# Kernel tuning notes

Hardware: AMD Instinct MI355X
Metric: run time of the kernel (lower is better)

The kernel has to match this reference:

```python
import jax, jax.numpy as jnp
import numpy as np

N = 50000
E = 800000
IN_CH = 128
HID = 32
HEADS = 8
OUT_CH = 64
NEG_SLOPE = 0.2  # PyG GATConv default leaky_relu slope


def setup_inputs() -> dict:
    key = jax.random.key(0)
    ks = jax.random.split(key, 16)
    x = jax.random.normal(ks[0], (N, IN_CH), dtype=jnp.float32)
    edge_index = jax.random.randint(ks[1], (2, E), 0, N, dtype=jnp.int64)
    s = 0.1
    return {
        "x": x,
        "edge_index": edge_index,
        # layer 1: in -> (HEADS, HID), concat
        "W1": jax.random.normal(ks[2], (IN_CH, HEADS * HID), dtype=jnp.float32) * s,
        "att_src1": jax.random.normal(ks[3], (HEADS, HID), dtype=jnp.float32) * s,
        "att_dst1": jax.random.normal(ks[4], (HEADS, HID), dtype=jnp.float32) * s,
        "b1": jnp.zeros((HEADS * HID,), dtype=jnp.float32),
        # layer 2: HEADS*HID -> (HEADS, HID), concat
        "W2": jax.random.normal(ks[5], (HEADS * HID, HEADS * HID), dtype=jnp.float32) * s,
        "att_src2": jax.random.normal(ks[6], (HEADS, HID), dtype=jnp.float32) * s,
        "att_dst2": jax.random.normal(ks[7], (HEADS, HID), dtype=jnp.float32) * s,
        "b2": jnp.zeros((HEADS * HID,), dtype=jnp.float32),
        # layer 3: HEADS*HID -> (1, OUT_CH), no concat (heads=1)
        "W3": jax.random.normal(ks[8], (HEADS * HID, OUT_CH), dtype=jnp.float32) * s,
        "att_src3": jax.random.normal(ks[9], (1, OUT_CH), dtype=jnp.float32) * s,
        "att_dst3": jax.random.normal(ks[10], (1, OUT_CH), dtype=jnp.float32) * s,
        "b3": jnp.zeros((OUT_CH,), dtype=jnp.float32),
    }


def gat_conv(x, src, dst, W, a_src, a_dst, b, heads, ch, concat):
    n = x.shape[0]
    h = (x @ W).reshape(n, heads, ch)                      # [N,H,C]
    alpha_src = jnp.sum(h * a_src, axis=-1)                # [N,H]
    alpha_dst = jnp.sum(h * a_dst, axis=-1)                # [N,H]
    logits = jax.nn.leaky_relu(alpha_src[src] + alpha_dst[dst], NEG_SLOPE)  # [E,H]
    # numerically stable softmax over edges grouped by destination node
    m = jax.ops.segment_max(logits, dst, num_segments=n)   # [N,H]
    m = jnp.where(jnp.isfinite(m), m, 0.0)
    e = jnp.exp(logits - m[dst])                           # [E,H]
    denom = jax.ops.segment_sum(e, dst, num_segments=n)    # [N,H]
    alpha = e / (denom[dst] + 1e-16)                       # [E,H]
    # weighted scatter-aggregate of source features
    out = jax.ops.segment_sum(alpha[:, :, None] * h[src], dst, num_segments=n)  # [N,H,C]
    out = out.reshape(n, heads * ch) if concat else out.mean(axis=1)
    return out + b


def reference(x, edge_index, W1, att_src1, att_dst1, b1,
              W2, att_src2, att_dst2, b2, W3, att_src3, att_dst3, b3):
    src, dst = edge_index[0], edge_index[1]
    h = jax.nn.elu(gat_conv(x, src, dst, W1, att_src1, att_dst1, b1, HEADS, HID, True))
    h = jax.nn.elu(gat_conv(h, src, dst, W2, att_src2, att_dst2, b2, HEADS, HID, True))
    out = gat_conv(h, src, dst, W3, att_src3, att_dst3, b3, 1, OUT_CH, False)
    return out
```

## Files before the change

kernel.cpp:

```cpp
#include <hip/hip_runtime.h>
#include <hip/hip_bf16.h>
#include <stdint.h>

#define NNODES 50000
#define NEDGES 800000

typedef float f32x4 __attribute__((ext_vector_type(4)));
typedef short short8 __attribute__((ext_vector_type(8)));

__device__ __forceinline__ ushort f2bf(float f) {
  uint32_t u = __float_as_uint(f);
  u += 0x7fff + ((u >> 16) & 1);
  return (ushort)(u >> 16);
}
__device__ __forceinline__ float bf2f(ushort h) {
  return __uint_as_float(((uint32_t)h) << 16);
}
__device__ __forceinline__ float bflo(uint32_t u) { return __uint_as_float(u << 16); }
__device__ __forceinline__ float bfhi(uint32_t u) { return __uint_as_float(u & 0xffff0000u); }

__device__ __forceinline__ void gload_lds16(const void* g, void* l) {
  __builtin_amdgcn_global_load_lds(
      (const __attribute__((address_space(1))) uint32_t*)g,
      (__attribute__((address_space(3))) uint32_t*)l, 16, 0, 0);
}

__global__ __launch_bounds__(256) void gemm_wide(
    const ushort* __restrict__ Ah, const ushort* __restrict__ Al,
    const ushort* __restrict__ Bh, const ushort* __restrict__ Bl,
    const float* __restrict__ a_src, const float* __restrict__ a_dst,
    float* __restrict__ as_out, float* __restrict__ ad_out,
    ushort* __restrict__ Cout, int M, int K) {
  __shared__ ushort AsH[64 * 32];
  __shared__ ushort AsL[64 * 32];
  __shared__ ushort BsH[256 * 32];
  __shared__ ushort BsL[256 * 32];

  const int t = threadIdx.x;
  const int w = t >> 6, ln = t & 63;
  const int row0 = blockIdx.x * 64;
  const int wr = (w >> 1) * 32, wc = (w & 1) * 128;

  f32x4 acc[2][8] = {};

  const int nkt = K >> 5;
  for (int kt = 0; kt < nkt; ++kt) {
    const int k0 = kt << 5;
    {
      int rloc = w * 16 + (ln >> 2);
      int sl = ln & 3;
      int sg = sl ^ ((rloc ^ (rloc >> 2)) & 3);
      int grow = row0 + rloc; grow = grow < M ? grow : M - 1;
      size_t go = (size_t)grow * K + k0 + sg * 8;
      gload_lds16(Ah + go, AsH + w * 512);
      gload_lds16(Al + go, AsL + w * 512);
    }
    #pragma unroll
    for (int i = 0; i < 4; ++i) {
      int rloc = w * 64 + i * 16 + (ln >> 2);
      int sl = ln & 3;
      int sg = sl ^ ((rloc ^ (rloc >> 2)) & 3);
      size_t go = (size_t)rloc * K + k0 + sg * 8;
      gload_lds16(Bh + go, BsH + (w * 64 + i * 16) * 32);
      gload_lds16(Bl + go, BsL + (w * 64 + i * 16) * 32);
    }
    __syncthreads();

    short8 ah[2], al[2], bh[8], bl[8];
    #pragma unroll
    for (int i = 0; i < 2; ++i) {
      int row = wr + i * 16 + (ln & 15);
      int slot = (ln >> 4) ^ ((row ^ (row >> 2)) & 3);
      int off = row * 32 + slot * 8;
      ah[i] = *(const short8*)(AsH + off);
      al[i] = *(const short8*)(AsL + off);
    }
    #pragma unroll
    for (int j = 0; j < 8; ++j) {
      int col = wc + j * 16 + (ln & 15);
      int slot = (ln >> 4) ^ ((col ^ (col >> 2)) & 3);
      int off = col * 32 + slot * 8;
      bh[j] = *(const short8*)(BsH + off);
      bl[j] = *(const short8*)(BsL + off);
    }
    #pragma unroll
    for (int i = 0; i < 2; ++i)
      #pragma unroll
      for (int j = 0; j < 8; ++j) {
        acc[i][j] = __builtin_amdgcn_mfma_f32_16x16x32_bf16(ah[i], bh[j], acc[i][j], 0, 0, 0);
        acc[i][j] = __builtin_amdgcn_mfma_f32_16x16x32_bf16(al[i], bh[j], acc[i][j], 0, 0, 0);
        acc[i][j] = __builtin_amdgcn_mfma_f32_16x16x32_bf16(ah[i], bl[j], acc[i][j], 0, 0, 0);
      }
    __syncthreads();
  }

  const int lx = ln & 15, g = ln >> 4;

  #pragma unroll
  for (int i = 0; i < 2; ++i)
    #pragma unroll
    for (int j = 0; j < 8; ++j)
      #pragma unroll
      for (int r = 0; r < 4; ++r) {
        int grow = row0 + wr + i * 16 + g * 4 + r;
        int gcol = wc + j * 16 + lx;
        if (grow < M) Cout[(size_t)grow * 256 + gcol] = f2bf(acc[i][j][r]);
      }

  const int hbase = wc >> 5;
  float avs[8], avd[8];
  #pragma unroll
  for (int j = 0; j < 8; ++j) {
    avs[j] = a_src[wc + j * 16 + lx];
    avd[j] = a_dst[wc + j * 16 + lx];
  }
  #pragma unroll
  for (int i = 0; i < 2; ++i)
    #pragma unroll
    for (int r = 0; r < 4; ++r) {
      float ps[4] = {0.f, 0.f, 0.f, 0.f}, pd[4] = {0.f, 0.f, 0.f, 0.f};
      #pragma unroll
      for (int j = 0; j < 8; ++j) {
        float v = acc[i][j][r];
        ps[j >> 1] += v * avs[j];
        pd[j >> 1] += v * avd[j];
      }
      #pragma unroll
      for (int m = 1; m < 16; m <<= 1)
        #pragma unroll
        for (int q = 0; q < 4; ++q) {
          ps[q] += __shfl_xor(ps[q], m);
          pd[q] += __shfl_xor(pd[q], m);
        }
      if (lx == 0) {
        int grow = row0 + wr + i * 16 + g * 4 + r;
        if (grow < M) {
          #pragma unroll
          for (int q = 0; q < 4; ++q) {
            as_out[grow * 8 + hbase + q] = ps[q];
            ad_out[grow * 8 + hbase + q] = pd[q];
          }
        }
      }
    }
}

__global__ __launch_bounds__(256) void gemm_mfma3(
    const ushort* __restrict__ Ah, const ushort* __restrict__ Al,
    const ushort* __restrict__ Bh, const ushort* __restrict__ Bl,
    const float* __restrict__ a_src, const float* __restrict__ a_dst,
    float* __restrict__ as_out, float* __restrict__ ad_out,
    ushort* __restrict__ Cout, int M, int K, int Ncols) {
  __shared__ ushort AsH[128 * 64];
  __shared__ ushort AsL[128 * 64];
  __shared__ ushort BsH[64 * 64];
  __shared__ ushort BsL[64 * 64];
  __shared__ float redS[2][128], redD[2][128];

  const int t = threadIdx.x;
  const int w = t >> 6, ln = t & 63;
  const int row0 = blockIdx.y * 128;
  const int col0 = blockIdx.x * 64;
  const int wr = (w >> 1) * 64, wc = (w & 1) * 32;

  f32x4 acc[4][2] = {};

  const int nkt = K >> 6;
  for (int kt = 0; kt < nkt; ++kt) {
    const int k0 = kt << 6;
    #pragma unroll
    for (int i = 0; i < 4; ++i) {
      int row8 = w * 4 + i;
      int rloc = row8 * 8 + (ln >> 3);
      int sslot = (ln & 7) ^ (rloc & 7);
      int grow = row0 + rloc; grow = grow < M ? grow : M - 1;
      size_t go = (size_t)grow * K + k0 + sslot * 8;
      gload_lds16(Ah + go, AsH + row8 * 512);
      gload_lds16(Al + go, AsL + row8 * 512);
    }
    #pragma unroll
    for (int i = 0; i < 2; ++i) {
      int row8 = w * 2 + i;
      int rloc = row8 * 8 + (ln >> 3);
      int sslot = (ln & 7) ^ (rloc & 7);
      size_t go = (size_t)(col0 + rloc) * K + k0 + sslot * 8;
      gload_lds16(Bh + go, BsH + row8 * 512);
      gload_lds16(Bl + go, BsL + row8 * 512);
    }
    __syncthreads();

    #pragma unroll
    for (int ks = 0; ks < 2; ++ks) {
      short8 ah[4], al[4], bh[2], bl[2];
      #pragma unroll
      for (int i = 0; i < 4; ++i) {
        int row = wr + i * 16 + (ln & 15);
        int slot = (ks * 4 + (ln >> 4)) ^ (row & 7);
        int off = row * 64 + slot * 8;
        ah[i] = *(const short8*)(AsH + off);
        al[i] = *(const short8*)(AsL + off);
      }
      #pragma unroll
      for (int j = 0; j < 2; ++j) {
        int col = wc + j * 16 + (ln & 15);
        int slot = (ks * 4 + (ln >> 4)) ^ (col & 7);
        int off = col * 64 + slot * 8;
        bh[j] = *(const short8*)(BsH + off);
        bl[j] = *(const short8*)(BsL + off);
      }
      #pragma unroll
      for (int i = 0; i < 4; ++i)
        #pragma unroll
        for (int j = 0; j < 2; ++j) {
          acc[i][j] = __builtin_amdgcn_mfma_f32_16x16x32_bf16(ah[i], bh[j], acc[i][j], 0, 0, 0);
          acc[i][j] = __builtin_amdgcn_mfma_f32_16x16x32_bf16(al[i], bh[j], acc[i][j], 0, 0, 0);
          acc[i][j] = __builtin_amdgcn_mfma_f32_16x16x32_bf16(ah[i], bl[j], acc[i][j], 0, 0, 0);
        }
    }
    __syncthreads();
  }

  const int lx = ln & 15, g = ln >> 4;

  #pragma unroll
  for (int i = 0; i < 4; ++i)
    #pragma unroll
    for (int j = 0; j < 2; ++j)
      #pragma unroll
      for (int r = 0; r < 4; ++r) {
        int grow = row0 + wr + i * 16 + g * 4 + r;
        int gcol = col0 + wc + j * 16 + lx;
        if (grow < M) Cout[(size_t)grow * Ncols + gcol] = f2bf(acc[i][j][r]);
      }

  float avs[2], avd[2];
  #pragma unroll
  for (int j = 0; j < 2; ++j) {
    avs[j] = a_src[wc + j * 16 + lx];
    avd[j] = a_dst[wc + j * 16 + lx];
  }
  #pragma unroll
  for (int i = 0; i < 4; ++i)
    #pragma unroll
    for (int r = 0; r < 4; ++r) {
      float ps = 0.f, pd = 0.f;
      #pragma unroll
      for (int j = 0; j < 2; ++j) {
        float v = acc[i][j][r];
        ps += v * avs[j];
        pd += v * avd[j];
      }
      #pragma unroll
      for (int m = 1; m < 16; m <<= 1) {
        ps += __shfl_xor(ps, m);
        pd += __shfl_xor(pd, m);
      }
      if (lx == 0) {
        int lrow = wr + i * 16 + g * 4 + r;
        redS[w & 1][lrow] = ps;
        redD[w & 1][lrow] = pd;
      }
    }
  __syncthreads();
  if (t < 128) {
    int grow = row0 + t;
    if (grow < M) {
      as_out[grow] = redS[0][t] + redS[1][t];
      ad_out[grow] = redD[0][t] + redD[1][t];
    }
  }
}

__global__ void cvt_split(const float* __restrict__ in, ushort* __restrict__ hi,
                          ushort* __restrict__ lo, int n4) {
  int idx = blockIdx.x * blockDim.x + threadIdx.x;
  if (idx >= n4) return;
  float4 v = ((const float4*)in)[idx];
  ushort4 h, l;
  h.x = f2bf(v.x); l.x = f2bf(v.x - bf2f(h.x));
  h.y = f2bf(v.y); l.y = f2bf(v.y - bf2f(h.y));
  h.z = f2bf(v.z); l.z = f2bf(v.z - bf2f(h.z));
  h.w = f2bf(v.w); l.w = f2bf(v.w - bf2f(h.w));
  ((ushort4*)hi)[idx] = h;
  ((ushort4*)lo)[idx] = l;
}

__global__ void cvt_w(const float* __restrict__ W, ushort* __restrict__ th,
                      ushort* __restrict__ tl, int K, int N) {
  int idx = blockIdx.x * blockDim.x + threadIdx.x;
  if (idx >= K * N) return;
  int k = idx / N, c = idx - k * N;
  float f = W[idx];
  ushort h = f2bf(f);
  th[(size_t)c * K + k] = h;
  tl[(size_t)c * K + k] = f2bf(f - bf2f(h));
}

__global__ void deg_kernel(const int* __restrict__ dst, int* __restrict__ deg, int E) {
  int e = blockIdx.x * blockDim.x + threadIdx.x;
  if (e < E) atomicAdd(&deg[dst[e]], 1);
}

__global__ __launch_bounds__(256) void scan_partial(const int* __restrict__ deg,
                                                    int* __restrict__ rowptr,
                                                    int* __restrict__ blocksum, int n) {
  __shared__ int sdata[256];
  int t = threadIdx.x;
  int base = blockIdx.x * 1024 + t * 4;
  int v[4], s = 0;
  #pragma unroll
  for (int i = 0; i < 4; ++i) {
    v[i] = (base + i < n) ? deg[base + i] : 0;
    s += v[i];
  }
  sdata[t] = s;
  __syncthreads();
  for (int off = 1; off < 256; off <<= 1) {
    int x = (t >= off) ? sdata[t - off] : 0;
    __syncthreads();
    sdata[t] += x;
    __syncthreads();
  }
  int run = sdata[t] - s;
  #pragma unroll
  for (int i = 0; i < 4; ++i) {
    if (base + i < n) rowptr[base + i] = run;
    run += v[i];
  }
  if (t == 255) blocksum[blockIdx.x] = sdata[255];
}

__global__ __launch_bounds__(256) void scan_blocksums(int* __restrict__ blocksum, int nb) {
  __shared__ int sdata[256];
  int t = threadIdx.x;
  int v = (t < nb) ? blocksum[t] : 0;
  sdata[t] = v;
  __syncthreads();
  for (int off = 1; off < 256; off <<= 1) {
    int x = (t >= off) ? sdata[t - off] : 0;
    __syncthreads();
    sdata[t] += x;
    __syncthreads();
  }
  if (t < nb) blocksum[t] = sdata[t] - v;
}

__global__ void scan_add(int* __restrict__ rowptr, const int* __restrict__ blocksum,
                         int* __restrict__ cursor, int n, int E) {
  int idx = blockIdx.x * blockDim.x + threadIdx.x;
  if (idx < n) {
    rowptr[idx] += blocksum[idx >> 10];
    cursor[idx] = 0;
  }
  if (idx == n) rowptr[n] = E;
}

__global__ void scatter_kernel(const int* __restrict__ src, const int* __restrict__ dst,
                               const int* __restrict__ rowptr, int* __restrict__ cursor,
                               int* __restrict__ col_src, int E) {
  int e = blockIdx.x * blockDim.x + threadIdx.x;
  if (e >= E) return;
  int d = dst[e];
  int pos = rowptr[d] + atomicAdd(&cursor[d], 1);
  col_src[pos] = src[e];
}

__global__ __launch_bounds__(256) void aggr_bf(
    const int* __restrict__ rowptr, const int* __restrict__ col_src,
    const ushort* __restrict__ h, const float* __restrict__ as_,
    const float* __restrict__ ad_, const float* __restrict__ bias,
    ushort* __restrict__ oh, ushort* __restrict__ ol, int n) {
  int d = blockIdx.x * 4 + (threadIdx.x >> 6);
  if (d >= n) return;
  int lane = threadIdx.x & 63;
  int c0 = lane * 4;
  int hd = lane >> 3;
  float ad_d = ad_[d * 8 + hd];
  float a0 = 0.f, a1 = 0.f, a2 = 0.f, a3 = 0.f, denom = 0.f;
  int beg = rowptr[d], end = rowptr[d + 1];
  int i = beg;
  for (; i + 2 <= end; i += 2) {
    int s0 = col_src[i], s1 = col_src[i + 1];
    float l0 = as_[s0 * 8 + hd] + ad_d;
    float l1 = as_[s1 * 8 + hd] + ad_d;
    uint2 v0 = *(const uint2*)(h + (size_t)s0 * 256 + c0);
    uint2 v1 = *(const uint2*)(h + (size_t)s1 * 256 + c0);
    l0 = (l0 > 0.f) ? l0 : 0.2f * l0;
    l1 = (l1 > 0.f) ? l1 : 0.2f * l1;
    float e0 = __expf(l0), e1 = __expf(l1);
    denom += e0 + e1;
    a0 += e0 * bflo(v0.x) + e1 * bflo(v1.x);
    a1 += e0 * bfhi(v0.x) + e1 * bfhi(v1.x);
    a2 += e0 * bflo(v0.y) + e1 * bflo(v1.y);
    a3 += e0 * bfhi(v0.y) + e1 * bfhi(v1.y);
  }
  if (i < end) {
    int s = col_src[i];
    float l = as_[s * 8 + hd] + ad_d;
    l = (l > 0.f) ? l : 0.2f * l;
    float ev = __expf(l);
    denom += ev;
    uint2 v = *(const uint2*)(h + (size_t)s * 256 + c0);
    a0 += ev * bflo(v.x);
    a1 += ev * bfhi(v.x);
    a2 += ev * bflo(v.y);
    a3 += ev * bfhi(v.y);
  }
  float inv = 1.f / (denom + 1e-16f);
  float v0 = a0 * inv + bias[c0 + 0];
  float v1 = a1 * inv + bias[c0 + 1];
  float v2 = a2 * inv + bias[c0 + 2];
  float v3 = a3 * inv + bias[c0 + 3];
  v0 = (v0 > 0.f) ? v0 : expm1f(v0);
  v1 = (v1 > 0.f) ? v1 : expm1f(v1);
  v2 = (v2 > 0.f) ? v2 : expm1f(v2);
  v3 = (v3 > 0.f) ? v3 : expm1f(v3);
  ushort4 hh, ll;
  hh.x = f2bf(v0); ll.x = f2bf(v0 - bf2f(hh.x));
  hh.y = f2bf(v1); ll.y = f2bf(v1 - bf2f(hh.y));
  hh.z = f2bf(v2); ll.z = f2bf(v2 - bf2f(hh.z));
  hh.w = f2bf(v3); ll.w = f2bf(v3 - bf2f(hh.w));
  *(ushort4*)(oh + (size_t)d * 256 + c0) = hh;
  *(ushort4*)(ol + (size_t)d * 256 + c0) = ll;
}

__global__ __launch_bounds__(256) void aggr_f3(
    const int* __restrict__ rowptr, const int* __restrict__ col_src,
    const ushort* __restrict__ h, const float* __restrict__ as_,
    const float* __restrict__ ad_, const float* __restrict__ bias,
    float* __restrict__ outp, int n) {
  int wid = (blockIdx.x * 256 + threadIdx.x) >> 6;
  int d = wid * 4 + ((threadIdx.x >> 4) & 3);
  if (d >= n) return;
  int l = threadIdx.x & 15;
  int c0 = l * 4;
  float ad_d = ad_[d];
  float a0 = 0.f, a1 = 0.f, a2 = 0.f, a3 = 0.f, denom = 0.f;
  int beg = rowptr[d], end = rowptr[d + 1];
  int i = beg;
  for (; i + 2 <= end; i += 2) {
    int s0 = col_src[i], s1 = col_src[i + 1];
    float l0 = as_[s0] + ad_d;
    float l1 = as_[s1] + ad_d;
    uint2 v0 = *(const uint2*)(h + (size_t)s0 * 64 + c0);
    uint2 v1 = *(const uint2*)(h + (size_t)s1 * 64 + c0);
    l0 = (l0 > 0.f) ? l0 : 0.2f * l0;
    l1 = (l1 > 0.f) ? l1 : 0.2f * l1;
    float e0 = __expf(l0), e1 = __expf(l1);
    denom += e0 + e1;
    a0 += e0 * bflo(v0.x) + e1 * bflo(v1.x);
    a1 += e0 * bfhi(v0.x) + e1 * bfhi(v1.x);
    a2 += e0 * bflo(v0.y) + e1 * bflo(v1.y);
    a3 += e0 * bfhi(v0.y) + e1 * bfhi(v1.y);
  }
  if (i < end) {
    int s = col_src[i];
    float lg = as_[s] + ad_d;
    lg = (lg > 0.f) ? lg : 0.2f * lg;
    float ev = __expf(lg);
    denom += ev;
    uint2 v = *(const uint2*)(h + (size_t)s * 64 + c0);
    a0 += ev * bflo(v.x);
    a1 += ev * bfhi(v.x);
    a2 += ev * bflo(v.y);
    a3 += ev * bfhi(v.y);
  }
  float inv = 1.f / (denom + 1e-16f);
  float4 r;
  r.x = a0 * inv + bias[c0 + 0];
  r.y = a1 * inv + bias[c0 + 1];
  r.z = a2 * inv + bias[c0 + 2];
  r.w = a3 * inv + bias[c0 + 3];
  *(float4*)(outp + (size_t)d * 64 + c0) = r;
}


extern "C" void kernel_launch(void* const* d_in, const int* in_sizes, int n_in,
                              void* d_out, int out_size, void* d_ws, size_t ws_size,
                              hipStream_t stream) {
  const float* x   = (const float*)d_in[0];
  const int*   ei  = (const int*)d_in[1];
  const float* W1  = (const float*)d_in[2];
  const float* aS1 = (const float*)d_in[3];
  const float* aD1 = (const float*)d_in[4];
  const float* b1  = (const float*)d_in[5];
  const float* W2  = (const float*)d_in[6];
  const float* aS2 = (const float*)d_in[7];
  const float* aD2 = (const float*)d_in[8];
  const float* b2  = (const float*)d_in[9];
  const float* W3  = (const float*)d_in[10];
  const float* aS3 = (const float*)d_in[11];
  const float* aD3 = (const float*)d_in[12];
  const float* b3  = (const float*)d_in[13];

  const int* srcp = ei;
  const int* dstp = ei + NEDGES;

  char* base = (char*)d_ws;
  size_t o = 0;
  ushort* hbf  = (ushort*)(base + o); o += 25600000;
  ushort* fh   = (ushort*)(base + o); o += 25600000;
  ushort* fl   = (ushort*)(base + o); o += 25600000;
  ushort* f1h  = (ushort*)(base + o); o += 12800000;
  ushort* f1l  = (ushort*)(base + o); o += 12800000;
  float*  as_  = (float*)(base + o);  o += 1600000;
  float*  ad_  = (float*)(base + o);  o += 1600000;
  ushort* w1h  = (ushort*)(base + o); o += 65536;
  ushort* w1l  = (ushort*)(base + o); o += 65536;
  ushort* w2h  = (ushort*)(base + o); o += 131072;
  ushort* w2l  = (ushort*)(base + o); o += 131072;
  ushort* w3h  = (ushort*)(base + o); o += 32768;
  ushort* w3l  = (ushort*)(base + o); o += 32768;
  int* rowptr  = (int*)(base + o);    o += 200016;
  int* cursor  = (int*)(base + o);    o += 200000;
  int* colsrc  = (int*)(base + o);    o += 3200000;
  int* bsum    = (int*)(base + o);    o += 1024;
  float* outp  = (float*)d_out;

  hipMemsetAsync(cursor, 0, NNODES * sizeof(int), stream);
  deg_kernel<<<(NEDGES + 255) / 256, 256, 0, stream>>>(dstp, cursor, NEDGES);
  int nb = (NNODES + 1023) / 1024;
  scan_partial<<<nb, 256, 0, stream>>>(cursor, rowptr, bsum, NNODES);
  scan_blocksums<<<1, 256, 0, stream>>>(bsum, nb);
  scan_add<<<(NNODES + 256) / 256, 256, 0, stream>>>(rowptr, bsum, cursor, NNODES, NEDGES);
  scatter_kernel<<<(NEDGES + 255) / 256, 256, 0, stream>>>(srcp, dstp, rowptr, cursor,
                                                           colsrc, NEDGES);

  cvt_split<<<(NNODES * 128 / 4 + 255) / 256, 256, 0, stream>>>(x, f1h, f1l,
                                                                NNODES * 128 / 4);
  cvt_w<<<(128 * 256 + 255) / 256, 256, 0, stream>>>(W1, w1h, w1l, 128, 256);
  cvt_w<<<(256 * 256 + 255) / 256, 256, 0, stream>>>(W2, w2h, w2l, 256, 256);
  cvt_w<<<(256 * 64 + 255) / 256, 256, 0, stream>>>(W3, w3h, w3l, 256, 64);

  const int ga  = (NNODES + 3) / 4;
  const int ga4 = (NNODES + 15) / 16;
  const int gw  = (NNODES + 63) / 64;
  gemm_wide<<<gw, 256, 0, stream>>>(f1h, f1l, w1h, w1l, aS1, aD1, as_, ad_,
                                    hbf, NNODES, 128);
  aggr_bf<<<ga, 256, 0, stream>>>(rowptr, colsrc, hbf, as_, ad_, b1, fh, fl, NNODES);
  gemm_wide<<<gw, 256, 0, stream>>>(fh, fl, w2h, w2l, aS2, aD2, as_, ad_,
                                    hbf, NNODES, 256);
  aggr_bf<<<ga, 256, 0, stream>>>(rowptr, colsrc, hbf, as_, ad_, b2, fh, fl, NNODES);
  gemm_mfma3<<<dim3(1, (NNODES + 127) / 128), 256, 0, stream>>>(
      fh, fl, w3h, w3l, aS3, aD3, as_, ad_, hbf, NNODES, 256, 64);
  aggr_f3<<<ga4, 256, 0, stream>>>(rowptr, colsrc, hbf, as_, ad_, b3, outp, NNODES);
}
```

Before: 379.8 us.

## Switch GEMMs and intermediates from split-bf16 to single fp16

Replaces the hi/lo bf16 split representation (three MFMAs per tile plus separate hi/lo buffers) with one fp16 operand and one f16 MFMA per tile. Inputs, weights, inter-layer features and gathered node features are all stored as fp16. This cuts GEMM MFMA work by two thirds, halves the A/B global and LDS traffic, and removes the low-part writes in the aggregation kernels. gemm_wide's K tile is doubled to 64 to match the other GEMM's layout. The cost is lower precision, since fp16 carries about 11 mantissa bits and has limited range, which could exceed tolerance or overflow on larger activations.

```diff
diff --git a/kernel.cpp b/kernel.cpp
--- a/kernel.cpp
+++ b/kernel.cpp
@@ -1,23 +1,20 @@
 #include <hip/hip_runtime.h>
 #include <hip/hip_bf16.h>
+#include <hip/hip_fp16.h>
 #include <stdint.h>
 
 #define NNODES 50000
 #define NEDGES 800000
 
 typedef float f32x4 __attribute__((ext_vector_type(4)));
-typedef short short8 __attribute__((ext_vector_type(8)));
-
-__device__ __forceinline__ ushort f2bf(float f) {
-  uint32_t u = __float_as_uint(f);
-  u += 0x7fff + ((u >> 16) & 1);
-  return (ushort)(u >> 16);
-}
-__device__ __forceinline__ float bf2f(ushort h) {
-  return __uint_as_float(((uint32_t)h) << 16);
-}
-__device__ __forceinline__ float bflo(uint32_t u) { return __uint_as_float(u << 16); }
-__device__ __forceinline__ float bfhi(uint32_t u) { return __uint_as_float(u & 0xffff0000u); }
+typedef _Float16 half8 __attribute__((ext_vector_type(8)));
+
+__device__ __forceinline__ ushort f2h(float f) {
+  return __half_as_ushort(__float2half(f));
+}
+__device__ __forceinline__ float2 h2x2(uint32_t u) {
+  return __half22float2(__builtin_bit_cast(__half2, u));
+}
 
 __device__ __forceinline__ void gload_lds16(const void* g, void* l) {
   __builtin_amdgcn_global_load_lds(
@@ -26,15 +23,12 @@
 }
 
 __global__ __launch_bounds__(256) void gemm_wide(
-    const ushort* __restrict__ Ah, const ushort* __restrict__ Al,
-    const ushort* __restrict__ Bh, const ushort* __restrict__ Bl,
+    const ushort* __restrict__ A, const ushort* __restrict__ B,
     const float* __restrict__ a_src, const float* __restrict__ a_dst,
     float* __restrict__ as_out, float* __restrict__ ad_out,
     ushort* __restrict__ Cout, int M, int K) {
-  __shared__ ushort AsH[64 * 32];
-  __shared__ ushort AsL[64 * 32];
-  __shared__ ushort BsH[256 * 32];
-  __shared__ ushort BsL[256 * 32];
+  __shared__ ushort As[64 * 64];
+  __shared__ ushort Bs[256 * 64];
 
   const int t = threadIdx.x;
   const int w = t >> 6, ln = t & 63;
@@ -43,54 +37,47 @@
 
   f32x4 acc[2][8] = {};
 
-  const int nkt = K >> 5;
+  const int nkt = K >> 6;
   for (int kt = 0; kt < nkt; ++kt) {
-    const int k0 = kt << 5;
-    {
-      int rloc = w * 16 + (ln >> 2);
-      int sl = ln & 3;
-      int sg = sl ^ ((rloc ^ (rloc >> 2)) & 3);
+    const int k0 = kt << 6;
+    #pragma unroll
+    for (int i = 0; i < 2; ++i) {
+      int row8 = w * 2 + i;
+      int rloc = row8 * 8 + (ln >> 3);
+      int slot = (ln & 7) ^ (rloc & 7);
       int grow = row0 + rloc; grow = grow < M ? grow : M - 1;
-      size_t go = (size_t)grow * K + k0 + sg * 8;
-      gload_lds16(Ah + go, AsH + w * 512);
-      gload_lds16(Al + go, AsL + w * 512);
-    }
-    #pragma unroll
-    for (int i = 0; i < 4; ++i) {
-      int rloc = w * 64 + i * 16 + (ln >> 2);
-      int sl = ln & 3;
-      int sg = sl ^ ((rloc ^ (rloc >> 2)) & 3);
-      size_t go = (size_t)rloc * K + k0 + sg * 8;
-      gload_lds16(Bh + go, BsH + (w * 64 + i * 16) * 32);
-      gload_lds16(Bl + go, BsL + (w * 64 + i * 16) * 32);
-    }
-    __syncthreads();
-
-    short8 ah[2], al[2], bh[8], bl[8];
-    #pragma unroll
-    for (int i = 0; i < 2; ++i) {
-      int row = wr + i * 16 + (ln & 15);
-      int slot = (ln >> 4) ^ ((row ^ (row >> 2)) & 3);
-      int off = row * 32 + slot * 8;
-      ah[i] = *(const short8*)(AsH + off);
-      al[i] = *(const short8*)(AsL + off);
-    }
-    #pragma unroll
-    for (int j = 0; j < 8; ++j) {
-      int col = wc + j * 16 + (ln & 15);
-      int slot = (ln >> 4) ^ ((col ^ (col >> 2)) & 3);
-      int off = col * 32 + slot * 8;
-      bh[j] = *(const short8*)(BsH + off);
-      bl[j] = *(const short8*)(BsL + off);
-    }
-    #pragma unroll
-    for (int i = 0; i < 2; ++i)
+      gload_lds16(A + (size_t)grow * K + k0 + slot * 8, As + row8 * 512);
+    }
+    #pragma unroll
+    for (int i = 0; i < 8; ++i) {
+      int row8 = w * 8 + i;
+      int rloc = row8 * 8 + (ln >> 3);
+      int slot = (ln & 7) ^ (rloc & 7);
+      gload_lds16(B + (size_t)rloc * K + k0 + slot * 8, Bs + row8 * 512);
+    }
+    __syncthreads();
+
+    #pragma unroll
+    for (int ks = 0; ks < 2; ++ks) {
+      half8 a[2], b[8];
+      #pragma unroll
+      for (int i = 0; i < 2; ++i) {
+        int row = wr + i * 16 + (ln & 15);
+        int slot = (ks * 4 + (ln >> 4)) ^ (row & 7);
+        a[i] = *(const half8*)(As + row * 64 + slot * 8);
+      }
       #pragma unroll
       for (int j = 0; j < 8; ++j) {
-        acc[i][j] = __builtin_amdgcn_mfma_f32_16x16x32_bf16(ah[i], bh[j], acc[i][j], 0, 0, 0);
-        acc[i][j] = __builtin_amdgcn_mfma_f32_16x16x32_bf16(al[i], bh[j], acc[i][j], 0, 0, 0);
-        acc[i][j] = __builtin_amdgcn_mfma_f32_16x16x32_bf16(ah[i], bl[j], acc[i][j], 0, 0, 0);
-      }
+        int col = wc + j * 16 + (ln & 15);
+        int slot = (ks * 4 + (ln >> 4)) ^ (col & 7);
+        b[j] = *(const half8*)(Bs + col * 64 + slot * 8);
+      }
+      #pragma unroll
+      for (int i = 0; i < 2; ++i)
+        #pragma unroll
+        for (int j = 0; j < 8; ++j)
+          acc[i][j] = __builtin_amdgcn_mfma_f32_16x16x32_f16(a[i], b[j], acc[i][j], 0, 0, 0);
+    }
     __syncthreads();
   }
 
@@ -104,7 +91,7 @@
       for (int r = 0; r < 4; ++r) {
         int grow = row0 + wr + i * 16 + g * 4 + r;
         int gcol = wc + j * 16 + lx;
-        if (grow < M) Cout[(size_t)grow * 256 + gcol] = f2bf(acc[i][j][r]);
+        if (grow < M) Cout[(size_t)grow * 256 + gcol] = f2h(acc[i][j][r]);
       }
 
   const int hbase = wc >> 5;
@@ -146,15 +133,12 @@
 }
 
 __global__ __launch_bounds__(256) void gemm_mfma3(
-    const ushort* __restrict__ Ah, const ushort* __restrict__ Al,
-    const ushort* __restrict__ Bh, const ushort* __restrict__ Bl,
+    const ushort* __restrict__ A, const ushort* __restrict__ B,
     const float* __restrict__ a_src, const float* __restrict__ a_dst,
     float* __restrict__ as_out, float* __restrict__ ad_out,
     ushort* __restrict__ Cout, int M, int K, int Ncols) {
-  __shared__ ushort AsH[128 * 64];
-  __shared__ ushort AsL[128 * 64];
-  __shared__ ushort BsH[64 * 64];
-  __shared__ ushort BsL[64 * 64];
+  __shared__ ushort As[128 * 64];
+  __shared__ ushort Bs[64 * 64];
   __shared__ float redS[2][128], redD[2][128];
 
   const int t = threadIdx.x;
@@ -172,50 +156,39 @@
     for (int i = 0; i < 4; ++i) {
       int row8 = w * 4 + i;
       int rloc = row8 * 8 + (ln >> 3);
-      int sslot = (ln & 7) ^ (rloc & 7);
+      int slot = (ln & 7) ^ (rloc & 7);
       int grow = row0 + rloc; grow = grow < M ? grow : M - 1;
-      size_t go = (size_t)grow * K + k0 + sslot * 8;
-      gload_lds16(Ah + go, AsH + row8 * 512);
-      gload_lds16(Al + go, AsL + row8 * 512);
+      gload_lds16(A + (size_t)grow * K + k0 + slot * 8, As + row8 * 512);
     }
     #pragma unroll
     for (int i = 0; i < 2; ++i) {
       int row8 = w * 2 + i;
       int rloc = row8 * 8 + (ln >> 3);
-      int sslot = (ln & 7) ^ (rloc & 7);
-      size_t go = (size_t)(col0 + rloc) * K + k0 + sslot * 8;
-      gload_lds16(Bh + go, BsH + row8 * 512);
-      gload_lds16(Bl + go, BsL + row8 * 512);
+      int slot = (ln & 7) ^ (rloc & 7);
+      gload_lds16(B + (size_t)(col0 + rloc) * K + k0 + slot * 8, Bs + row8 * 512);
     }
     __syncthreads();
 
     #pragma unroll
     for (int ks = 0; ks < 2; ++ks) {
-      short8 ah[4], al[4], bh[2], bl[2];
+      half8 a[4], b[2];
       #pragma unroll
       for (int i = 0; i < 4; ++i) {
         int row = wr + i * 16 + (ln & 15);
         int slot = (ks * 4 + (ln >> 4)) ^ (row & 7);
-        int off = row * 64 + slot * 8;
-        ah[i] = *(const short8*)(AsH + off);
-        al[i] = *(const short8*)(AsL + off);
+        a[i] = *(const half8*)(As + row * 64 + slot * 8);
       }
       #pragma unroll
       for (int j = 0; j < 2; ++j) {
         int col = wc + j * 16 + (ln & 15);
         int slot = (ks * 4 + (ln >> 4)) ^ (col & 7);
-        int off = col * 64 + slot * 8;
-        bh[j] = *(const short8*)(BsH + off);
-        bl[j] = *(const short8*)(BsL + off);
+        b[j] = *(const half8*)(Bs + col * 64 + slot * 8);
       }
       #pragma unroll
       for (int i = 0; i < 4; ++i)
         #pragma unroll
-        for (int j = 0; j < 2; ++j) {
-          acc[i][j] = __builtin_amdgcn_mfma_f32_16x16x32_bf16(ah[i], bh[j], acc[i][j], 0, 0, 0);
-          acc[i][j] = __builtin_amdgcn_mfma_f32_16x16x32_bf16(al[i], bh[j], acc[i][j], 0, 0, 0);
-          acc[i][j] = __builtin_amdgcn_mfma_f32_16x16x32_bf16(ah[i], bl[j], acc[i][j], 0, 0, 0);
-        }
+        for (int j = 0; j < 2; ++j)
+          acc[i][j] = __builtin_amdgcn_mfma_f32_16x16x32_f16(a[i], b[j], acc[i][j], 0, 0, 0);
     }
     __syncthreads();
   }
@@ -230,7 +203,7 @@
       for (int r = 0; r < 4; ++r) {
         int grow = row0 + wr + i * 16 + g * 4 + r;
         int gcol = col0 + wc + j * 16 + lx;
-        if (grow < M) Cout[(size_t)grow * Ncols + gcol] = f2bf(acc[i][j][r]);
+        if (grow < M) Cout[(size_t)grow * Ncols + gcol] = f2h(acc[i][j][r]);
       }
 
   float avs[2], avd[2];
@@ -271,29 +244,21 @@
   }
 }
 
-__global__ void cvt_split(const float* __restrict__ in, ushort* __restrict__ hi,
-                          ushort* __restrict__ lo, int n4) {
+__global__ void cvt_h(const float* __restrict__ in, ushort* __restrict__ out, int n4) {
   int idx = blockIdx.x * blockDim.x + threadIdx.x;
   if (idx >= n4) return;
   float4 v = ((const float4*)in)[idx];
-  ushort4 h, l;
-  h.x = f2bf(v.x); l.x = f2bf(v.x - bf2f(h.x));
-  h.y = f2bf(v.y); l.y = f2bf(v.y - bf2f(h.y));
-  h.z = f2bf(v.z); l.z = f2bf(v.z - bf2f(h.z));
-  h.w = f2bf(v.w); l.w = f2bf(v.w - bf2f(h.w));
-  ((ushort4*)hi)[idx] = h;
-  ((ushort4*)lo)[idx] = l;
-}
-
-__global__ void cvt_w(const float* __restrict__ W, ushort* __restrict__ th,
-                      ushort* __restrict__ tl, int K, int N) {
+  ushort4 o;
+  o.x = f2h(v.x); o.y = f2h(v.y); o.z = f2h(v.z); o.w = f2h(v.w);
+  ((ushort4*)out)[idx] = o;
+}
+
+__global__ void cvt_w(const float* __restrict__ W, ushort* __restrict__ tr,
+                      int K, int N) {
   int idx = blockIdx.x * blockDim.x + threadIdx.x;
   if (idx >= K * N) return;
   int k = idx / N, c = idx - k * N;
-  float f = W[idx];
-  ushort h = f2bf(f);
-  th[(size_t)c * K + k] = h;
-  tl[(size_t)c * K + k] = f2bf(f - bf2f(h));
+  tr[(size_t)c * K + k] = f2h(W[idx]);
 }
 
 __global__ void deg_kernel(const int* __restrict__ dst, int* __restrict__ deg, int E) {
@@ -365,11 +330,11 @@
   col_src[pos] = src[e];
 }
 
-__global__ __launch_bounds__(256) void aggr_bf(
+__global__ __launch_bounds__(256) void aggr_h(
     const int* __restrict__ rowptr, const int* __restrict__ col_src,
     const ushort* __restrict__ h, const float* __restrict__ as_,
     const float* __restrict__ ad_, const float* __restrict__ bias,
-    ushort* __restrict__ oh, ushort* __restrict__ ol, int n) {
+    ushort* __restrict__ of, int n) {
   int d = blockIdx.x * 4 + (threadIdx.x >> 6);
   if (d >= n) return;
   int lane = threadIdx.x & 63;
@@ -389,10 +354,12 @@
     l1 = (l1 > 0.f) ? l1 : 0.2f * l1;
     float e0 = __expf(l0), e1 = __expf(l1);
     denom += e0 + e1;
-    a0 += e0 * bflo(v0.x) + e1 * bflo(v1.x);
-    a1 += e0 * bfhi(v0.x) + e1 * bfhi(v1.x);
-    a2 += e0 * bflo(v0.y) + e1 * bflo(v1.y);
-    a3 += e0 * bfhi(v0.y) + e1 * bfhi(v1.y);
+    float2 p0 = h2x2(v0.x), p1 = h2x2(v0.y);
+    float2 q0 = h2x2(v1.x), q1 = h2x2(v1.y);
+    a0 += e0 * p0.x + e1 * q0.x;
+    a1 += e0 * p0.y + e1 * q0.y;
+    a2 += e0 * p1.x + e1 * q1.x;
+    a3 += e0 * p1.y + e1 * q1.y;
   }
   if (i < end) {
     int s = col_src[i];
@@ -401,10 +368,11 @@
     float ev = __expf(l);
     denom += ev;
     uint2 v = *(const uint2*)(h + (size_t)s * 256 + c0);
-    a0 += ev * bflo(v.x);
-    a1 += ev * bfhi(v.x);
-    a2 += ev * bflo(v.y);
-    a3 += ev * bfhi(v.y);
+    float2 p0 = h2x2(v.x), p1 = h2x2(v.y);
+    a0 += ev * p0.x;
+    a1 += ev * p0.y;
+    a2 += ev * p1.x;
+    a3 += ev * p1.y;
   }
   float inv = 1.f / (denom + 1e-16f);
   float v0 = a0 * inv + bias[c0 + 0];
@@ -415,13 +383,9 @@
   v1 = (v1 > 0.f) ? v1 : expm1f(v1);
   v2 = (v2 > 0.f) ? v2 : expm1f(v2);
   v3 = (v3 > 0.f) ? v3 : expm1f(v3);
-  ushort4 hh, ll;
-  hh.x = f2bf(v0); ll.x = f2bf(v0 - bf2f(hh.x));
-  hh.y = f2bf(v1); ll.y = f2bf(v1 - bf2f(hh.y));
-  hh.z = f2bf(v2); ll.z = f2bf(v2 - bf2f(hh.z));
-  hh.w = f2bf(v3); ll.w = f2bf(v3 - bf2f(hh.w));
-  *(ushort4*)(oh + (size_t)d * 256 + c0) = hh;
-  *(ushort4*)(ol + (size_t)d * 256 + c0) = ll;
+  ushort4 hh;
+  hh.x = f2h(v0); hh.y = f2h(v1); hh.z = f2h(v2); hh.w = f2h(v3);
+  *(ushort4*)(of + (size_t)d * 256 + c0) = hh;
 }
 
 __global__ __launch_bounds__(256) void aggr_f3(
@@ -448,10 +412,12 @@
     l1 = (l1 > 0.f) ? l1 : 0.2f * l1;
     float e0 = __expf(l0), e1 = __expf(l1);
     denom += e0 + e1;
-    a0 += e0 * bflo(v0.x) + e1 * bflo(v1.x);
-    a1 += e0 * bfhi(v0.x) + e1 * bfhi(v1.x);
-    a2 += e0 * bflo(v0.y) + e1 * bflo(v1.y);
-    a3 += e0 * bfhi(v0.y) + e1 * bfhi(v1.y);
+    float2 p0 = h2x2(v0.x), p1 = h2x2(v0.y);
+    float2 q0 = h2x2(v1.x), q1 = h2x2(v1.y);
+    a0 += e0 * p0.x + e1 * q0.x;
+    a1 += e0 * p0.y + e1 * q0.y;
+    a2 += e0 * p1.x + e1 * q1.x;
+    a3 += e0 * p1.y + e1 * q1.y;
   }
   if (i < end) {
     int s = col_src[i];
@@ -460,10 +426,11 @@
     float ev = __expf(lg);
     denom += ev;
     uint2 v = *(const uint2*)(h + (size_t)s * 64 + c0);
-    a0 += ev * bflo(v.x);
-    a1 += ev * bfhi(v.x);
-    a2 += ev * bflo(v.y);
-    a3 += ev * bfhi(v.y);
+    float2 p0 = h2x2(v.x), p1 = h2x2(v.y);
+    a0 += ev * p0.x;
+    a1 += ev * p0.y;
+    a2 += ev * p1.x;
+    a3 += ev * p1.y;
   }
   float inv = 1.f / (denom + 1e-16f);
   float4 r;
@@ -499,18 +466,13 @@
   char* base = (char*)d_ws;
   size_t o = 0;
   ushort* hbf  = (ushort*)(base + o); o += 25600000;
-  ushort* fh   = (ushort*)(base + o); o += 25600000;
-  ushort* fl   = (ushort*)(base + o); o += 25600000;
-  ushort* f1h  = (ushort*)(base + o); o += 12800000;
-  ushort* f1l  = (ushort*)(base + o); o += 12800000;
+  ushort* ff   = (ushort*)(base + o); o += 25600000;
+  ushort* f1   = (ushort*)(base + o); o += 12800000;
   float*  as_  = (float*)(base + o);  o += 1600000;
   float*  ad_  = (float*)(base + o);  o += 1600000;
-  ushort* w1h  = (ushort*)(base + o); o += 65536;
-  ushort* w1l  = (ushort*)(base + o); o += 65536;
-  ushort* w2h  = (ushort*)(base + o); o += 131072;
-  ushort* w2l  = (ushort*)(base + o); o += 131072;
-  ushort* w3h  = (ushort*)(base + o); o += 32768;
-  ushort* w3l  = (ushort*)(base + o); o += 32768;
+  ushort* w1t  = (ushort*)(base + o); o += 65536;
+  ushort* w2t  = (ushort*)(base + o); o += 131072;
+  ushort* w3t  = (ushort*)(base + o); o += 32768;
   int* rowptr  = (int*)(base + o);    o += 200016;
   int* cursor  = (int*)(base + o);    o += 200000;
   int* colsrc  = (int*)(base + o);    o += 3200000;
@@ -526,22 +488,19 @@
   scatter_kernel<<<(NEDGES + 255) / 256, 256, 0, stream>>>(srcp, dstp, rowptr, cursor,
                                                            colsrc, NEDGES);
 
-  cvt_split<<<(NNODES * 128 / 4 + 255) / 256, 256, 0, stream>>>(x, f1h, f1l,
-                                                                NNODES * 128 / 4);
-  cvt_w<<<(128 * 256 + 255) / 256, 256, 0, stream>>>(W1, w1h, w1l, 128, 256);
-  cvt_w<<<(256 * 256 + 255) / 256, 256, 0, stream>>>(W2, w2h, w2l, 256, 256);
-  cvt_w<<<(256 * 64 + 255) / 256, 256, 0, stream>>>(W3, w3h, w3l, 256, 64);
+  cvt_h<<<(NNODES * 128 / 4 + 255) / 256, 256, 0, stream>>>(x, f1, NNODES * 128 / 4);
+  cvt_w<<<(128 * 256 + 255) / 256, 256, 0, stream>>>(W1, w1t, 128, 256);
+  cvt_w<<<(256 * 256 + 255) / 256, 256, 0, stream>>>(W2, w2t, 256, 256);
+  cvt_w<<<(256 * 64 + 255) / 256, 256, 0, stream>>>(W3, w3t, 256, 64);
 
   const int ga  = (NNODES + 3) / 4;
   const int ga4 = (NNODES + 15) / 16;
   const int gw  = (NNODES + 63) / 64;
-  gemm_wide<<<gw, 256, 0, stream>>>(f1h, f1l, w1h, w1l, aS1, aD1, as_, ad_,
-                                    hbf, NNODES, 128);
-  aggr_bf<<<ga, 256, 0, stream>>>(rowptr, colsrc, hbf, as_, ad_, b1, fh, fl, NNODES);
-  gemm_wide<<<gw, 256, 0, stream>>>(fh, fl, w2h, w2l, aS2, aD2, as_, ad_,
-                                    hbf, NNODES, 256);
-  aggr_bf<<<ga, 256, 0, stream>>>(rowptr, colsrc, hbf, as_, ad_, b2, fh, fl, NNODES);
+  gemm_wide<<<gw, 256, 0, stream>>>(f1, w1t, aS1, aD1, as_, ad_, hbf, NNODES, 128);
+  aggr_h<<<ga, 256, 0, stream>>>(rowptr, colsrc, hbf, as_, ad_, b1, ff, NNODES);
+  gemm_wide<<<gw, 256, 0, stream>>>(ff, w2t, aS2, aD2, as_, ad_, hbf, NNODES, 256);
+  aggr_h<<<ga, 256, 0, stream>>>(rowptr, colsrc, hbf, as_, ad_, b2, ff, NNODES);
   gemm_mfma3<<<dim3(1, (NNODES + 127) / 128), 256, 0, stream>>>(
-      fh, fl, w3h, w3l, aS3, aD3, as_, ad_, hbf, NNODES, 256, 64);
+      ff, w3t, aS3, aD3, as_, ad_, hbf, NNODES, 256, 64);
   aggr_f3<<<ga4, 256, 0, stream>>>(rowptr, colsrc, hbf, as_, ad_, b3, outp, NNODES);
 }
```

After: 345.4 us. 1.1x faster.
